# Kernel tuning notes

Hardware: AMD Instinct MI355X
Metric: run time of the kernel (lower is better)

Reference implementation:

```python
import jax, jax.numpy as jnp
import numpy as np

# Geometry constants fixed by the source's index arithmetic
GRID_P, GRID_Q, NUM_ANCH = 60, 40, 9   # p = (i//9)%60, q = i//(60*9), sr = i%9
N = GRID_P * GRID_Q * NUM_ANCH          # 21600 anchors per image
K = 1000                                # top-K candidates kept before NMS
MAX_BOXES = 18                          # fixed output boxes per image
THRESH = 0.5                            # NMS overlap threshold
BATCH = 64


def setup_inputs() -> dict:
    key = jax.random.key(0)
    k1, k2 = jax.random.split(key)
    x = jax.random.normal(k1, (BATCH, N, 6), dtype=jnp.float32)
    # anchor boxes (x, y, w, h); keep w,h strictly positive and away from 0
    anchor_boxes = jax.random.uniform(k2, (GRID_P, GRID_Q, NUM_ANCH, 4),
                                      dtype=jnp.float32, minval=0.05, maxval=1.0)
    return {"x": x, "anchor_boxes": anchor_boxes}


def _per_sample(ypred, anchors):
    scores, order = jax.lax.top_k(ypred[:, 0], K)          # descending, matches tf.argsort DESC [:1000]
    p = (order // NUM_ANCH) % GRID_P
    q = order // (GRID_P * NUM_ANCH)
    sr = order % NUM_ANCH
    a = anchors[p, q, sr]                                   # [K, 4] (xa, ya, wa, ha)
    regr = ypred[order, 2:6]                                # [K, 4] (dx, dy, dw, dh)
    xc = regr[:, 0] * a[:, 2] + a[:, 0]
    yc = regr[:, 1] * a[:, 3] + a[:, 1]
    w = a[:, 2] * jnp.exp(regr[:, 2])
    h = a[:, 3] * jnp.exp(regr[:, 3])
    cand = jnp.stack([xc, yc, w, h, scores], axis=-1)       # [K, 5] xywh+score

    # xywh -> xyxy for overlap computation (as in non_max_suppression_fast)
    x1 = xc - 0.5 * w; x2 = xc + 0.5 * w
    y1 = yc - 0.5 * h; y2 = yc + 0.5 * h
    area = (x2 - x1) * (y2 - y1)                            # [K]

    # pairwise intersection; overlap[i, j] = inter(i, j) / area(j)  (source divides by
    # the area of the lower-scored candidate, NOT the union -- kept faithfully)
    xx1 = jnp.maximum(x1[:, None], x1[None, :])
    yy1 = jnp.maximum(y1[:, None], y1[None, :])
    xx2 = jnp.minimum(x2[:, None], x2[None, :])
    yy2 = jnp.minimum(y2[:, None], y2[None, :])
    iw = jnp.maximum(0.0, xx2 - xx1)
    ih = jnp.maximum(0.0, yy2 - yy1)
    sup = (iw * ih / area[None, :]) > THRESH                # [K, K] bool

    # greedy NMS over candidates in descending-score order
    jrange = jnp.arange(K)
    def body(i, keep):
        return keep & ~(keep[i] & sup[i] & (jrange > i))
    keep = jax.lax.fori_loop(0, K, body, jnp.ones((K,), dtype=bool))

    # pack first MAX_BOXES kept boxes into fixed-shape output
    ranks = jnp.cumsum(keep) - 1                            # position among kept
    valid = keep & (ranks < MAX_BOXES)
    picked = jnp.zeros((MAX_BOXES, 5), cand.dtype).at[
        jnp.where(valid, ranks, MAX_BOXES)
    ].set(jnp.where(valid[:, None], cand, 0.0), mode='drop')

    # pad with top-scored decoded boxes if fewer than MAX_BOXES survive NMS
    n = jnp.minimum(jnp.sum(keep), MAX_BOXES)
    j = jnp.arange(MAX_BOXES)
    pad = cand[jnp.clip(j - n, 0, K - 1)]
    return jnp.where((j < n)[:, None], picked, pad)         # [MAX_BOXES, 5]


def reference(x, anchor_boxes):
    return jax.vmap(lambda y: _per_sample(y, anchor_boxes))(x)  # [B, 18, 5]
```

## Files before the change

### kernel.cpp

```cpp
#include <hip/hip_runtime.h>

#define NELEM 21600
#define KSEL 1000
#define MAXB 18
#define NT 1024
#define CAP 2048
#define NCHUNK 4
#define CHUNK (NELEM / NCHUNK)
#define NFULL 21
#define NTAIL (NELEM - NFULL * NT)

typedef unsigned long long ull;

__device__ __forceinline__ unsigned fkey(float f) {
  unsigned u = __float_as_uint(f);
  return (u & 0x80000000u) ? ~u : (u | 0x80000000u);
}
__device__ __forceinline__ float unfkey(unsigned k) {
  unsigned u = (k & 0x80000000u) ? (k ^ 0x80000000u) : ~k;
  return __uint_as_float(u);
}

__global__ __launch_bounds__(NT) void k1_scan(
    const float* __restrict__ x, unsigned* __restrict__ gkeys,
    unsigned* __restrict__ ghist) {
  const int blk = blockIdx.x;
  const int s = blk / NCHUNK, c = blk % NCHUNK;
  const int t = threadIdx.x;
  const float* xb = x + (size_t)s * NELEM * 6;

  __shared__ unsigned h[2048];
  h[2 * t] = 0u; h[2 * t + 1] = 0u;
  __syncthreads();

  const int base = c * CHUNK;
  unsigned key[6];
  bool on[6];
  #pragma unroll
  for (int k = 0; k < 6; ++k) {
    int o = t + (k << 10);
    on[k] = o < CHUNK;
    int e = base + (on[k] ? o : 0);
    key[k] = fkey(xb[(size_t)e * 6]);
  }
  #pragma unroll
  for (int k = 0; k < 6; ++k) {
    if (on[k]) {
      int e = base + t + (k << 10);
      gkeys[(size_t)s * NELEM + e] = key[k];
      atomicAdd(&h[key[k] >> 21], 1u);
    }
  }
  __syncthreads();
  unsigned* gh = ghist + (size_t)blk * 2048;
  gh[2 * t] = h[2 * t];
  gh[2 * t + 1] = h[2 * t + 1];
}

__device__ void select_bucket(const unsigned* hist, unsigned target,
                              volatile unsigned* chunkSuf,
                              unsigned* outB, unsigned* outCnt, unsigned* outAbove) {
  const int tid = threadIdx.x;
  const int w = tid >> 6, l = tid & 63;
  unsigned h1 = hist[w * 128 + 2 * l + 1];
  unsigned s = hist[w * 128 + 2 * l] + h1;
  #pragma unroll
  for (int d = 1; d < 64; d <<= 1) {
    unsigned t = __shfl_down(s, d);
    if (l + d < 64) s += t;
  }
  if (l == 0) chunkSuf[w] = s;
  __syncthreads();
  if (w == 0) {
    unsigned ct = (l < 16) ? chunkSuf[l] : 0u;
    unsigned cs = ct;
    #pragma unroll
    for (int d = 1; d < 16; d <<= 1) {
      unsigned t = __shfl_down(cs, d);
      if (l + d < 16) cs += t;
    }
    if (l < 16) chunkSuf[l] = cs - ct;
  }
  __syncthreads();
  unsigned base = chunkSuf[w];
  unsigned sufE = s + base;
  unsigned sN = __shfl_down(s, 1);
  unsigned sufN = ((l < 63) ? sN : 0u) + base;
  unsigned geOdd = sufN + h1;
  if (sufE >= target && geOdd < target) { *outB = w * 128u + 2u * l;     *outCnt = sufE;  *outAbove = geOdd; }
  if (geOdd >= target && sufN < target) { *outB = w * 128u + 2u * l + 1; *outCnt = geOdd; *outAbove = sufN;  }
  __syncthreads();
}

__global__ __launch_bounds__(NT, 4) void k2_select(
    const float* __restrict__ x, const float* __restrict__ anch,
    const unsigned* __restrict__ gkeys, const unsigned* __restrict__ ghist,
    float* __restrict__ out) {
  const int s = blockIdx.x;
  const int tid = threadIdx.x;
  const float* xb = x + (size_t)s * NELEM * 6;
  const unsigned* ks = gkeys + (size_t)s * NELEM;

  __shared__ unsigned hist[2048];
  __shared__ unsigned chunkSuf[16];
  __shared__ ull selPk[CAP];
  __shared__ float bX1[KSEL], bY1[KSEL], bX2[KSEL], bY2[KSEL], bAr[KSEL];
  __shared__ unsigned sB, sCnt, sAbove;
  __shared__ unsigned baseKey;
  __shared__ unsigned cnt;
  __shared__ int keptRank[MAXB];
  __shared__ int numKept;

  unsigned kv[NFULL];
  #pragma unroll
  for (int u = 0; u < NFULL; ++u) kv[u] = ks[tid + (u << 10)];
  unsigned ktail = 0u;
  const bool hastail = tid < NTAIL;
  if (hastail) ktail = ks[tid + NFULL * NT];
  asm volatile("" :
      "+v"(kv[0]), "+v"(kv[1]), "+v"(kv[2]), "+v"(kv[3]), "+v"(kv[4]),
      "+v"(kv[5]), "+v"(kv[6]), "+v"(kv[7]), "+v"(kv[8]), "+v"(kv[9]),
      "+v"(kv[10]), "+v"(kv[11]), "+v"(kv[12]), "+v"(kv[13]), "+v"(kv[14]),
      "+v"(kv[15]), "+v"(kv[16]), "+v"(kv[17]), "+v"(kv[18]), "+v"(kv[19]),
      "+v"(kv[20]), "+v"(ktail));

  {
    unsigned h0 = 0, h1 = 0;
    #pragma unroll
    for (int c = 0; c < NCHUNK; ++c) {
      const unsigned* gh = ghist + (size_t)(s * NCHUNK + c) * 2048;
      h0 += gh[2 * tid];
      h1 += gh[2 * tid + 1];
    }
    hist[2 * tid] = h0; hist[2 * tid + 1] = h1;
  }
  __syncthreads();
  select_bucket(hist, KSEL, chunkSuf, &sB, &sCnt, &sAbove);
  const unsigned b1 = sB, cnt1 = sCnt, above1 = sAbove;

  if (cnt1 > 1024) {
    hist[2 * tid] = 0u; hist[2 * tid + 1] = 0u;
    __syncthreads();
    #pragma unroll
    for (int u = 0; u < NFULL; ++u)
      if ((kv[u] >> 21) == b1) atomicAdd(&hist[(kv[u] >> 10) & 0x7FFu], 1u);
    if (hastail && (ktail >> 21) == b1) atomicAdd(&hist[(ktail >> 10) & 0x7FFu], 1u);
    __syncthreads();
    select_bucket(hist, KSEL - above1, chunkSuf, &sB, &sCnt, &sAbove);
    if (tid == 0) { baseKey = (b1 << 21) | (sB << 10); cnt = 0u; }
  } else {
    if (tid == 0) { baseKey = b1 << 21; cnt = 0u; }
  }
  __syncthreads();

  const unsigned TB = baseKey;
  const int lw = tid & 63;
  #pragma unroll
  for (int u = 0; u < NFULL; ++u) {
    bool pred = kv[u] >= TB;
    ull mask = __ballot(pred);
    if (mask) {
      int leader = __builtin_ctzll(mask);
      unsigned total = (unsigned)__popcll(mask);
      unsigned basep = 0;
      if (lw == leader) basep = atomicAdd(&cnt, total);
      basep = __shfl(basep, leader);
      if (pred) {
        unsigned p = basep + (unsigned)__popcll(mask & ((1ull << lw) - 1ull));
        unsigned i = (unsigned)(tid + (u << 10));
        if (p < CAP) selPk[p] = ((ull)kv[u] << 32) | (unsigned)(~i);
      }
    }
  }
  if (hastail && ktail >= TB) {
    unsigned p = atomicAdd(&cnt, 1u);
    unsigned i = (unsigned)(tid + NFULL * NT);
    if (p < CAP) selPk[p] = ((ull)ktail << 32) | (unsigned)(~i);
  }
  __syncthreads();
  const unsigned realCnt = (cnt < CAP) ? cnt : CAP;
  const unsigned P = (realCnt <= 1024u) ? 1024u : 2048u;
  for (unsigned i = realCnt + tid; i < P; i += NT) selPk[i] = 0ull;
  __syncthreads();

  if (P == 1024u) {
    ull a = selPk[tid];
    #pragma unroll
    for (unsigned k = 2; k <= 64; k <<= 1) {
      #pragma unroll
      for (unsigned j = k >> 1; j >= 1; j >>= 1) {
        bool up = ((tid & k) == 0);
        bool lower = ((tid & j) == 0);
        bool takeMax = (up == lower);
        ull o = __shfl_xor(a, (int)j);
        a = takeMax ? (a > o ? a : o) : (a < o ? a : o);
      }
    }
    selPk[tid] = a;
    __syncthreads();
    for (unsigned k = 128; k <= 1024; k <<= 1) {
      for (unsigned j = k >> 1; j >= 64; j >>= 1) {
        if (tid < 512) {
          unsigned p = (unsigned)tid;
          unsigned vi = ((p & ~(j - 1)) << 1) | (p & (j - 1));
          unsigned li = vi | j;
          ull av = selPk[vi], cv = selPk[li];
          bool doswap = ((vi & k) == 0) ? (av < cv) : (av > cv);
          if (doswap) { selPk[vi] = cv; selPk[li] = av; }
        }
        __syncthreads();
      }
      a = selPk[tid];
      {
        bool up = ((tid & k) == 0);
        #pragma unroll
        for (unsigned j = 32; j >= 1; j >>= 1) {
          bool lower = ((tid & j) == 0);
          bool takeMax = (up == lower);
          ull o = __shfl_xor(a, (int)j);
          a = takeMax ? (a > o ? a : o) : (a < o ? a : o);
        }
      }
      selPk[tid] = a;
      __syncthreads();
    }
  } else {
    const int w = tid >> 6, L = tid & 63;
    const int ea = (w << 7) | (L << 1);
    ull a = selPk[ea], bb = selPk[ea + 1];
    #pragma unroll
    for (unsigned k = 2; k <= 128; k <<= 1) {
      #pragma unroll
      for (unsigned j = k >> 1; j >= 2; j >>= 1) {
        bool up = ((ea & k) == 0);
        bool lower = ((ea & j) == 0);
        bool takeMax = (up == lower);
        ull oa = __shfl_xor(a, (int)(j >> 1));
        ull ob = __shfl_xor(bb, (int)(j >> 1));
        a  = takeMax ? (a  > oa ? a  : oa) : (a  < oa ? a  : oa);
        bb = takeMax ? (bb > ob ? bb : ob) : (bb < ob ? bb : ob);
      }
      bool up = ((ea & k) == 0);
      ull mx = a > bb ? a : bb, mn = a > bb ? bb : a;
      a = up ? mx : mn; bb = up ? mn : mx;
    }
    selPk[ea] = a; selPk[ea + 1] = bb;
    __syncthreads();
    for (unsigned k = 256; k <= 2048; k <<= 1) {
      for (unsigned j = k >> 1; j >= 128; j >>= 1) {
        unsigned p = (unsigned)tid;
        unsigned vi = ((p & ~(j - 1)) << 1) | (p & (j - 1));
        unsigned li = vi | j;
        ull av = selPk[vi], cv = selPk[li];
        bool doswap = ((vi & k) == 0) ? (av < cv) : (av > cv);
        if (doswap) { selPk[vi] = cv; selPk[li] = av; }
        __syncthreads();
      }
      a = selPk[ea]; bb = selPk[ea + 1];
      bool up = (((unsigned)(w << 7) & k) == 0);
      #pragma unroll
      for (unsigned j = 64; j >= 2; j >>= 1) {
        bool lower = ((ea & j) == 0);
        bool takeMax = (up == lower);
        ull oa = __shfl_xor(a, (int)(j >> 1));
        ull ob = __shfl_xor(bb, (int)(j >> 1));
        a  = takeMax ? (a  > oa ? a  : oa) : (a  < oa ? a  : oa);
        bb = takeMax ? (bb > ob ? bb : ob) : (bb < ob ? bb : ob);
      }
      ull mx = a > bb ? a : bb, mn = a > bb ? bb : a;
      a = up ? mx : mn; bb = up ? mn : mx;
      selPk[ea] = a; selPk[ea + 1] = bb;
      __syncthreads();
    }
  }

  if (tid < KSEL) {
    unsigned idx = ~(unsigned)selPk[tid];
    const float2* e2 = (const float2*)(xb + (size_t)idx * 6 + 2);
    float2 ra = e2[0], rb = e2[1];
    unsigned pp = (idx / 9u) % 60u;
    unsigned qq = idx / 540u;
    unsigned sr = idx % 9u;
    const float* ap = anch + (((pp * 40u + qq) * 9u + sr) * 4u);
    float ax = ap[0], ay = ap[1], aw = ap[2], ah = ap[3];
    float xc = ra.x * aw + ax;
    float yc = ra.y * ah + ay;
    float w = aw * expf(rb.x);
    float h = ah * expf(rb.y);
    float x1 = xc - 0.5f * w, x2 = xc + 0.5f * w;
    float y1 = yc - 0.5f * h, y2 = yc + 0.5f * h;
    bX1[tid] = x1; bY1[tid] = y1; bX2[tid] = x2; bY2[tid] = y2;
    bAr[tid] = (x2 - x1) * (y2 - y1);
  }
  __syncthreads();

  if (tid < 64) {
    const int lane = tid;
    float X1[16], Y1[16], X2[16], Y2[16], AR[16];
    unsigned alive = 0u;
    #pragma unroll
    for (int ss = 0; ss < 16; ++ss) {
      int r = lane * 16 + ss;
      bool ok = r < KSEL;
      int rr = ok ? r : 0;
      X1[ss] = bX1[rr]; Y1[ss] = bY1[rr];
      X2[ss] = bX2[rr]; Y2[ss] = bY2[rr]; AR[ss] = bAr[rr];
      alive |= (ok ? 1u : 0u) << ss;
    }
    int nk = 0;
    while (nk < MAXB) {
      int local = alive ? (lane * 16 + (int)__builtin_ctz(alive)) : (1 << 30);
      int m = local;
      #pragma unroll
      for (int d = 1; d < 64; d <<= 1) {
        int o = __shfl_xor(m, d);
        m = o < m ? o : m;
      }
      if (m >= (1 << 30)) break;
      if (lane == 0) keptRank[nk] = m;
      float wx1 = bX1[m], wy1 = bY1[m], wx2 = bX2[m], wy2 = bY2[m];
      ++nk;
      if (alive) {
        #pragma unroll
        for (int ss = 0; ss < 16; ++ss) {
          if (alive & (1u << ss)) {
            float iw = fmaxf(fminf(X2[ss], wx2) - fmaxf(X1[ss], wx1), 0.f);
            float ih = fmaxf(fminf(Y2[ss], wy2) - fmaxf(Y1[ss], wy1), 0.f);
            if (iw * ih / AR[ss] > 0.5f) alive &= ~(1u << ss);
          }
        }
      }
    }
    if (lane == 0) numKept = nk;
  }
  __syncthreads();

  const int n = numKept;
  if (tid < MAXB) {
    int j = tid;
    int r = (j < n) ? keptRank[j] : (j - n);
    ull pk = selPk[r];
    unsigned idx = ~(unsigned)pk;
    float sc = unfkey((unsigned)(pk >> 32));
    const float2* e2 = (const float2*)(xb + (size_t)idx * 6 + 2);
    float2 ra = e2[0], rb = e2[1];
    unsigned pp = (idx / 9u) % 60u;
    unsigned qq = idx / 540u;
    unsigned sr = idx % 9u;
    const float* ap = anch + (((pp * 40u + qq) * 9u + sr) * 4u);
    float ax = ap[0], ay = ap[1], aw = ap[2], ah = ap[3];
    float xc = ra.x * aw + ax;
    float yc = ra.y * ah + ay;
    float w = aw * expf(rb.x);
    float h = ah * expf(rb.y);
    float* o = out + s * (MAXB * 5) + j * 5;
    o[0] = xc; o[1] = yc; o[2] = w; o[3] = h; o[4] = sc;
  }
}

extern "C" void kernel_launch(void* const* d_in, const int* in_sizes, int n_in,
                              void* d_out, int out_size, void* d_ws, size_t ws_size,
                              hipStream_t stream) {
  const float* x = (const float*)d_in[0];
  const float* anch = (const float*)d_in[1];
  float* out = (float*)d_out;
  const int B = in_sizes[0] / (NELEM * 6);
  unsigned* ghist = (unsigned*)d_ws;
  unsigned* gkeys = ghist + (size_t)B * NCHUNK * 2048;
  k1_scan<<<dim3(B * NCHUNK), dim3(NT), 0, stream>>>(x, gkeys, ghist);
  k2_select<<<dim3(B), dim3(NT), 0, stream>>>(x, anch, gkeys, ghist, out);
}
```

Before: 60.93 us.

## Vectorize key scan, split select kernel into sort and NMS kernels

The scan kernel now reads the input as float4 and takes scores from the .x or .z lane, so each anchor's score comes out of a wide load instead of a strided scalar load. The former select kernel is split into a sort kernel, which writes the sorted packed keys to workspace, and a separate NMS kernel with lower register and LDS pressure. The NMS kernel pads its shared arrays to stride 17 to avoid bank conflicts and finds the next winner with a ballot plus one shuffle instead of a six-step shuffle reduction. The cost is an extra launch and a global round trip of the sorted keys.

```diff
diff --git a/kernel.cpp b/kernel.cpp
--- a/kernel.cpp
+++ b/kernel.cpp
@@ -6,7 +6,7 @@
 #define NT 1024
 #define CAP 2048
 #define NCHUNK 4
-#define CHUNK (NELEM / NCHUNK)
+#define QC 8100
 #define NFULL 21
 #define NTAIL (NELEM - NFULL * NT)
 
@@ -27,28 +27,41 @@
   const int blk = blockIdx.x;
   const int s = blk / NCHUNK, c = blk % NCHUNK;
   const int t = threadIdx.x;
-  const float* xb = x + (size_t)s * NELEM * 6;
+  const float4* xq = (const float4*)(x + (size_t)s * NELEM * 6);
+  unsigned* gk = gkeys + (size_t)s * NELEM;
 
   __shared__ unsigned h[2048];
   h[2 * t] = 0u; h[2 * t + 1] = 0u;
   __syncthreads();
 
-  const int base = c * CHUNK;
-  unsigned key[6];
-  bool on[6];
+  const int base = c * QC;
   #pragma unroll
-  for (int k = 0; k < 6; ++k) {
-    int o = t + (k << 10);
-    on[k] = o < CHUNK;
-    int e = base + (on[k] ? o : 0);
-    key[k] = fkey(xb[(size_t)e * 6]);
-  }
-  #pragma unroll
-  for (int k = 0; k < 6; ++k) {
-    if (on[k]) {
-      int e = base + t + (k << 10);
-      gkeys[(size_t)s * NELEM + e] = key[k];
-      atomicAdd(&h[key[k] >> 21], 1u);
+  for (int k = 0; k < 7; ++k) {
+    int g = base + t + (k << 10);
+    float4 v = xq[g];
+    int r = g % 3;
+    if (r == 0) {
+      unsigned key = fkey(v.x);
+      gk[2 * (g / 3)] = key;
+      atomicAdd(&h[key >> 21], 1u);
+    } else if (r == 1) {
+      unsigned key = fkey(v.z);
+      gk[2 * (g / 3) + 1] = key;
+      atomicAdd(&h[key >> 21], 1u);
+    }
+  }
+  if (t < QC - 7 * 1024) {
+    int g = base + t + (7 << 10);
+    float4 v = xq[g];
+    int r = g % 3;
+    if (r == 0) {
+      unsigned key = fkey(v.x);
+      gk[2 * (g / 3)] = key;
+      atomicAdd(&h[key >> 21], 1u);
+    } else if (r == 1) {
+      unsigned key = fkey(v.z);
+      gk[2 * (g / 3) + 1] = key;
+      atomicAdd(&h[key >> 21], 1u);
     }
   }
   __syncthreads();
@@ -92,24 +105,19 @@
   __syncthreads();
 }
 
-__global__ __launch_bounds__(NT, 4) void k2_select(
-    const float* __restrict__ x, const float* __restrict__ anch,
+__global__ __launch_bounds__(NT, 4) void k2a_sort(
     const unsigned* __restrict__ gkeys, const unsigned* __restrict__ ghist,
-    float* __restrict__ out) {
+    ull* __restrict__ gsort) {
   const int s = blockIdx.x;
   const int tid = threadIdx.x;
-  const float* xb = x + (size_t)s * NELEM * 6;
   const unsigned* ks = gkeys + (size_t)s * NELEM;
 
   __shared__ unsigned hist[2048];
   __shared__ unsigned chunkSuf[16];
   __shared__ ull selPk[CAP];
-  __shared__ float bX1[KSEL], bY1[KSEL], bX2[KSEL], bY2[KSEL], bAr[KSEL];
   __shared__ unsigned sB, sCnt, sAbove;
   __shared__ unsigned baseKey;
   __shared__ unsigned cnt;
-  __shared__ int keptRank[MAXB];
-  __shared__ int numKept;
 
   unsigned kv[NFULL];
   #pragma unroll
@@ -274,8 +282,25 @@
     }
   }
 
+  gsort[(size_t)s * 1024 + tid] = selPk[tid];
+}
+
+__global__ __launch_bounds__(NT, 2) void k2b_nms(
+    const float* __restrict__ x, const float* __restrict__ anch,
+    const ull* __restrict__ gsort, float* __restrict__ out) {
+  const int s = blockIdx.x;
+  const int tid = threadIdx.x;
+  const float* xb = x + (size_t)s * NELEM * 6;
+
+  __shared__ ull pkL[1024];
+  __shared__ float px1[64 * 17], py1[64 * 17], px2[64 * 17], py2[64 * 17], par[64 * 17];
+  __shared__ int keptRank[MAXB];
+  __shared__ int numKept;
+
+  ull pk = gsort[(size_t)s * 1024 + tid];
+  pkL[tid] = pk;
   if (tid < KSEL) {
-    unsigned idx = ~(unsigned)selPk[tid];
+    unsigned idx = ~(unsigned)pk;
     const float2* e2 = (const float2*)(xb + (size_t)idx * 6 + 2);
     float2 ra = e2[0], rb = e2[1];
     unsigned pp = (idx / 9u) % 60u;
@@ -289,8 +314,9 @@
     float h = ah * expf(rb.y);
     float x1 = xc - 0.5f * w, x2 = xc + 0.5f * w;
     float y1 = yc - 0.5f * h, y2 = yc + 0.5f * h;
-    bX1[tid] = x1; bY1[tid] = y1; bX2[tid] = x2; bY2[tid] = y2;
-    bAr[tid] = (x2 - x1) * (y2 - y1);
+    int a = (tid >> 4) * 17 + (tid & 15);
+    px1[a] = x1; py1[a] = y1; px2[a] = x2; py2[a] = y2;
+    par[a] = (x2 - x1) * (y2 - y1);
   }
   __syncthreads();
 
@@ -301,33 +327,30 @@
     #pragma unroll
     for (int ss = 0; ss < 16; ++ss) {
       int r = lane * 16 + ss;
-      bool ok = r < KSEL;
-      int rr = ok ? r : 0;
-      X1[ss] = bX1[rr]; Y1[ss] = bY1[rr];
-      X2[ss] = bX2[rr]; Y2[ss] = bY2[rr]; AR[ss] = bAr[rr];
-      alive |= (ok ? 1u : 0u) << ss;
+      int a = lane * 17 + ss;
+      X1[ss] = px1[a]; Y1[ss] = py1[a];
+      X2[ss] = px2[a]; Y2[ss] = py2[a]; AR[ss] = par[a];
+      alive |= (r < KSEL ? 1u : 0u) << ss;
     }
     int nk = 0;
     while (nk < MAXB) {
-      int local = alive ? (lane * 16 + (int)__builtin_ctz(alive)) : (1 << 30);
-      int m = local;
+      ull bal = __ballot(alive != 0u);
+      if (!bal) break;
+      int F = __builtin_ctzll(bal);
+      int myss = (int)__builtin_ctz(alive | 0x10000u);
+      int ssw = __shfl(myss, F);
+      int m = F * 16 + ssw;
+      if (lane == 0) keptRank[nk] = m;
+      int am = (m >> 4) * 17 + (m & 15);
+      float wx1 = px1[am], wy1 = py1[am], wx2 = px2[am], wy2 = py2[am];
+      ++nk;
+      if (nk >= MAXB) break;
       #pragma unroll
-      for (int d = 1; d < 64; d <<= 1) {
-        int o = __shfl_xor(m, d);
-        m = o < m ? o : m;
-      }
-      if (m >= (1 << 30)) break;
-      if (lane == 0) keptRank[nk] = m;
-      float wx1 = bX1[m], wy1 = bY1[m], wx2 = bX2[m], wy2 = bY2[m];
-      ++nk;
-      if (alive) {
-        #pragma unroll
-        for (int ss = 0; ss < 16; ++ss) {
-          if (alive & (1u << ss)) {
-            float iw = fmaxf(fminf(X2[ss], wx2) - fmaxf(X1[ss], wx1), 0.f);
-            float ih = fmaxf(fminf(Y2[ss], wy2) - fmaxf(Y1[ss], wy1), 0.f);
-            if (iw * ih / AR[ss] > 0.5f) alive &= ~(1u << ss);
-          }
+      for (int ss = 0; ss < 16; ++ss) {
+        if (alive & (1u << ss)) {
+          float iw = fmaxf(fminf(X2[ss], wx2) - fmaxf(X1[ss], wx1), 0.f);
+          float ih = fmaxf(fminf(Y2[ss], wy2) - fmaxf(Y1[ss], wy1), 0.f);
+          if (iw * ih / AR[ss] > 0.5f) alive &= ~(1u << ss);
         }
       }
     }
@@ -339,9 +362,9 @@
   if (tid < MAXB) {
     int j = tid;
     int r = (j < n) ? keptRank[j] : (j - n);
-    ull pk = selPk[r];
-    unsigned idx = ~(unsigned)pk;
-    float sc = unfkey((unsigned)(pk >> 32));
+    ull pkr = pkL[r];
+    unsigned idx = ~(unsigned)pkr;
+    float sc = unfkey((unsigned)(pkr >> 32));
     const float2* e2 = (const float2*)(xb + (size_t)idx * 6 + 2);
     float2 ra = e2[0], rb = e2[1];
     unsigned pp = (idx / 9u) % 60u;
@@ -367,6 +390,8 @@
   const int B = in_sizes[0] / (NELEM * 6);
   unsigned* ghist = (unsigned*)d_ws;
   unsigned* gkeys = ghist + (size_t)B * NCHUNK * 2048;
+  ull* gsort = (ull*)(gkeys + (size_t)B * NELEM);
   k1_scan<<<dim3(B * NCHUNK), dim3(NT), 0, stream>>>(x, gkeys, ghist);
-  k2_select<<<dim3(B), dim3(NT), 0, stream>>>(x, anch, gkeys, ghist, out);
-}
+  k2a_sort<<<dim3(B), dim3(NT), 0, stream>>>(gkeys, ghist, gsort);
+  k2b_nms<<<dim3(B), dim3(NT), 0, stream>>>(x, anch, gsort, out);
+}
```

Measured after the change: 58.68 us. -3.7%, faster.
